# Optimization experiments

Hardware: AMD Instinct MI355X
Metric: run time of the kernel (lower is better)

Reference implementation:

```python
import jax, jax.numpy as jnp
import numpy as np

# regular 3x3 kernel grid: row0 = dy (i-1), row1 = dx (j-1), k = 3*i + j
RY = jnp.array([-1., -1., -1., 0., 0., 0., 1., 1., 1.], dtype=jnp.float32)
RX = jnp.array([-1., 0., 1., -1., 0., 1., -1., 0., 1.], dtype=jnp.float32)


def conv2d(x, w, b):
    # 3x3, stride 1, pad 1, NCHW/OIHW
    out = jax.lax.conv_general_dilated(
        x, w, window_strides=(1, 1), padding=((1, 1), (1, 1)),
        dimension_numbers=('NCHW', 'OIHW', 'NCHW'))
    return out + b[None, :, None, None]


def group_norm(x, gamma, beta, num_groups, eps=1e-5):
    N, C, H, W = x.shape
    xg = x.reshape(N, num_groups, C // num_groups, H, W)
    mu = xg.mean(axis=(2, 3, 4), keepdims=True)
    var = xg.var(axis=(2, 3, 4), keepdims=True)
    xn = ((xg - mu) * jax.lax.rsqrt(var + eps)).reshape(N, C, H, W)
    return xn * gamma[None, :, None, None] + beta[None, :, None, None]


def build_offset(tm, tr):
    # tm: [N,4,H,W] per-pixel 2x2 affine [[m00,m01],[m10,m11]]; tr: [N,2,H,W] (ty, tx)
    m00, m01, m10, m11 = tm[:, 0], tm[:, 1], tm[:, 2], tm[:, 3]  # [N,H,W]
    ry = RY[None, :, None, None]
    rx = RX[None, :, None, None]
    # offset = M @ R - R, plus translation broadcast to all 9 points
    dy = m00[:, None] * ry + m01[:, None] * rx - ry + tr[:, 0:1]  # [N,9,H,W]
    dx = m10[:, None] * ry + m11[:, None] * rx - rx + tr[:, 1:2]  # [N,9,H,W]
    return dy, dx


def bilinear_sample(img, py, px):
    # img: [N,C,H,W]; py, px: [N,K,H,W] sampling locations; zero padding outside
    N, C, H, W = img.shape
    K = py.shape[1]
    y0f = jnp.floor(py)
    x0f = jnp.floor(px)
    wy1 = py - y0f
    wx1 = px - x0f
    wy0 = 1.0 - wy1
    wx0 = 1.0 - wx1
    y0 = y0f.astype(jnp.int32)
    x0 = x0f.astype(jnp.int32)
    img_flat = img.reshape(N, C, H * W)

    def gather(yi, xi):
        valid = ((yi >= 0) & (yi < H) & (xi >= 0) & (xi < W)).astype(img.dtype)
        idx = jnp.clip(yi, 0, H - 1) * W + jnp.clip(xi, 0, W - 1)  # [N,K,H,W]
        flat = idx.reshape(N, 1, K * H * W)
        vals = jnp.take_along_axis(img_flat, jnp.broadcast_to(flat, (N, C, K * H * W)), axis=2)
        return vals.reshape(N, C, K, H, W) * valid[:, None]

    v00 = gather(y0, x0)
    v01 = gather(y0, x0 + 1)
    v10 = gather(y0 + 1, x0)
    v11 = gather(y0 + 1, x0 + 1)
    return (v00 * (wy0 * wx0)[:, None] + v01 * (wy0 * wx1)[:, None]
            + v10 * (wy1 * wx0)[:, None] + v11 * (wy1 * wx1)[:, None])


def deform_conv(x, dy, dx, w, pad=1, dil=1):
    # x: [N,Cin,H,W]; dy,dx: [N,9,H,W]; w: [Cout,Cin,3,3]; stride 1
    N, C, H, W = x.shape
    k = jnp.arange(9)
    ki = (k // 3).astype(x.dtype)[None, :, None, None]
    kj = (k % 3).astype(x.dtype)[None, :, None, None]
    hh = jnp.arange(H, dtype=x.dtype)[None, None, :, None]
    ww = jnp.arange(W, dtype=x.dtype)[None, None, None, :]
    py = hh - pad + dil * ki + dy  # [N,9,H,W]
    px = ww - pad + dil * kj + dx
    sampled = bilinear_sample(x, py, px)  # [N,C,9,H,W]
    return jnp.einsum('nckhw,ock->nohw', sampled, w.reshape(w.shape[0], C, 9))


def setup_inputs() -> dict:
    key = jax.random.key(0)
    ks = jax.random.split(key, 16)
    N, C, H, W = 4, 256, 64, 64
    x = jax.random.normal(ks[0], (N, C, H, W), jnp.float32)
    def p(k, shape, s):
        return jax.random.normal(k, shape, jnp.float32) * s
    s_off = 0.01                       # small STN heads -> modest offsets
    s_dc = 1.0 / np.sqrt(C * 9.0)      # deform-conv fan-in init
    return {
        'x': x,
        'w_tm1': p(ks[1], (4, C, 3, 3), s_off), 'b_tm1': jnp.zeros((4,), jnp.float32),
        'w_tr1': p(ks[2], (2, C, 3, 3), s_off), 'b_tr1': jnp.zeros((2,), jnp.float32),
        'w_dc1': p(ks[3], (C, C, 3, 3), s_dc),
        'g1': jnp.ones((C,), jnp.float32), 'be1': jnp.zeros((C,), jnp.float32),
        'w_tm2': p(ks[4], (4, C, 3, 3), s_off), 'b_tm2': jnp.zeros((4,), jnp.float32),
        'w_tr2': p(ks[5], (2, C, 3, 3), s_off), 'b_tr2': jnp.zeros((2,), jnp.float32),
        'w_dc2': p(ks[6], (C, C, 3, 3), s_dc),
        'g2': jnp.ones((C,), jnp.float32), 'be2': jnp.zeros((C,), jnp.float32),
    }


def reference(x, w_tm1, b_tm1, w_tr1, b_tr1, w_dc1, g1, be1,
              w_tm2, b_tm2, w_tr2, b_tr2, w_dc2, g2, be2):
    GROUPS = 32
    residual = x
    dy1, dx1 = build_offset(conv2d(x, w_tm1, b_tm1), conv2d(x, w_tr1, b_tr1))
    out = deform_conv(x, dy1, dx1, w_dc1)
    out = jax.nn.relu(group_norm(out, g1, be1, GROUPS))
    dy2, dx2 = build_offset(conv2d(out, w_tm2, b_tm2), conv2d(out, w_tr2, b_tr2))
    out = deform_conv(out, dy2, dx2, w_dc2)
    out = group_norm(out, g2, be2, GROUPS)
    return jax.nn.relu(out + residual)
```

## Files before the change

### kernel.cpp

```cpp
#include <hip/hip_runtime.h>


typedef unsigned int u32;
typedef unsigned short u16;
typedef __attribute__((ext_vector_type(8))) short bf16x8;
typedef __attribute__((ext_vector_type(4))) float floatx4;

#define HW 4096
#define CHW 1048576

static __device__ __forceinline__ float bf2f(u16 u) {
    union { u32 i; float f; } c; c.i = ((u32)u) << 16; return c.f;
}
static __device__ __forceinline__ u16 f2bf(float f) {
    union { float f; u32 i; } c; c.f = f;
    u32 x = c.i;
    return (u16)((x + 0x7FFFu + ((x >> 16) & 1u)) >> 16);
}
static __device__ __forceinline__ u32 cvtpk(float a, float b) {
    u32 r;
    asm("v_cvt_pk_bf16_f32 %0, %1, %2" : "=v"(r) : "v"(a), "v"(b));
    return r;
}
static __device__ __forceinline__ void lbar() {
    __builtin_amdgcn_sched_barrier(0);
    asm volatile("s_waitcnt lgkmcnt(0)" ::: "memory");
    __builtin_amdgcn_s_barrier();
    __builtin_amdgcn_sched_barrier(0);
}
static __device__ __forceinline__ float loadv(const void* p, long i, int f32) {
    return f32 ? ((const float*)p)[i] : bf2f(((const u16*)p)[i]);
}
static __device__ __forceinline__ int sniff_f32(const u32* __restrict__ xw) {
    int cnt = 0;
    #pragma unroll
    for (int s = 0; s < 16; ++s) {
        union { u32 i; float f; } c;
        c.i = xw[s * 131 + 7];
        float a = fabsf(c.f);
        if (a > 1e-8f && a < 1e4f) ++cnt;
    }
    return (cnt >= 8) ? 1 : 0;
}

__global__ __launch_bounds__(256) void k_prep_all(
    const void* __restrict__ x,
    const void* __restrict__ wdc1, const void* __restrict__ wdc2,
    const void* __restrict__ wtm1, const void* __restrict__ wtr1,
    const void* __restrict__ wtm2, const void* __restrict__ wtr2,
    u16* __restrict__ xT, u16* __restrict__ wTg1, u16* __restrict__ wTg2,
    u16* __restrict__ wT61, u16* __restrict__ wT62)
{
    __shared__ u16 T[64 * 258];
    const int f32 = sniff_f32((const u32*)x);
    const int b = blockIdx.x;
    const int tid = threadIdx.x;

    if (b < 256) {
        const int n = b >> 6, h = b & 63;
        const long sb = (long)n * CHW + (h << 6);
        const int cb = tid >> 3;
        const int w0 = (tid & 7) << 3;
        if (f32) {
            const float* xp = (const float*)x;
            for (int it = 0; it < 8; ++it) {
                int c = (it << 5) + cb;
                const float* pr = xp + sb + (long)c * HW + w0;
                float4 a = ((const float4*)pr)[0];
                float4 d = ((const float4*)pr)[1];
                T[(w0 + 0) * 258 + c] = f2bf(a.x);
                T[(w0 + 1) * 258 + c] = f2bf(a.y);
                T[(w0 + 2) * 258 + c] = f2bf(a.z);
                T[(w0 + 3) * 258 + c] = f2bf(a.w);
                T[(w0 + 4) * 258 + c] = f2bf(d.x);
                T[(w0 + 5) * 258 + c] = f2bf(d.y);
                T[(w0 + 6) * 258 + c] = f2bf(d.z);
                T[(w0 + 7) * 258 + c] = f2bf(d.w);
            }
        } else {
            const u16* xp = (const u16*)x;
            for (int it = 0; it < 8; ++it) {
                int c = (it << 5) + cb;
                uint4 v = *(const uint4*)(xp + sb + (long)c * HW + w0);
                u32 ws[4] = {v.x, v.y, v.z, v.w};
                #pragma unroll
                for (int q = 0; q < 4; ++q) {
                    T[(w0 + 2 * q + 0) * 258 + c] = (u16)(ws[q] & 0xFFFFu);
                    T[(w0 + 2 * q + 1) * 258 + c] = (u16)(ws[q] >> 16);
                }
            }
        }
        __syncthreads();
        const int w = tid >> 2, cq = tid & 3;
        const u32* Tr = (const u32*)T;
        u16* ob = xT + (long)n * CHW + (long)((h << 6) + w) * 256 + cq * 64;
        #pragma unroll
        for (int s = 0; s < 8; ++s) {
            uint4 o;
            o.x = Tr[129 * w + 32 * cq + 4 * s + 0];
            o.y = Tr[129 * w + 32 * cq + 4 * s + 1];
            o.z = Tr[129 * w + 32 * cq + 4 * s + 2];
            o.w = Tr[129 * w + 32 * cq + 4 * s + 3];
            *(uint4*)&ob[s * 8] = o;
        }
    } else if (b < 2560) {
        const int r2 = (b >= 1408);
        const void* wdc = r2 ? wdc2 : wdc1;
        u16* wTg = r2 ? wTg2 : wTg1;
        int idx2 = (b - (r2 ? 1408 : 256)) * 256 + tid;
        int cp = idx2 & 15;
        int o  = (idx2 >> 4) & 255;
        int q  = idx2 >> 12;
        int k  = q >> 3;
        int c0 = ((q & 7) << 5) + (cp << 1);
        long s0 = (long)o * 2304 + c0 * 9 + k;
        ((u32*)wTg)[idx2] = cvtpk(loadv(wdc, s0, f32), loadv(wdc, s0 + 9, f32));
    } else {
        const int r2 = (b >= 2704);
        const void* wtm = r2 ? wtm2 : wtm1;
        const void* wtr = r2 ? wtr2 : wtr1;
        u16* wT6 = r2 ? wT62 : wT61;
        int i = (b - (r2 ? 2704 : 2560)) * 256 + tid;
        int q  = i >> 9;
        int o  = (i >> 5) & 15;
        int cc = i & 31;
        int k  = q >> 3;
        int c  = ((q & 7) << 5) + cc;
        float v = 0.f;
        if (o < 4)      v = loadv(wtm, (long)o * 2304 + c * 9 + k, f32);
        else if (o < 6) v = loadv(wtr, (long)(o - 4) * 2304 + c * 9 + k, f32);
        wT6[i] = f2bf(v);
    }
}

__global__ __launch_bounds__(1024, 4) void k_deform(
    const u16* __restrict__ srcT, const u16* __restrict__ wTg,
    const u16* __restrict__ wT6,
    const void* __restrict__ b_tm, const void* __restrict__ b_tr,
    const u32* __restrict__ xw,
    u16* __restrict__ raw, float* __restrict__ pstats)
{
    __shared__ __align__(16) char shm[65536];
    __shared__ float tl[6 * 64];
    __shared__ int   g_y0[576];
    __shared__ int   g_x0[576];
    __shared__ float g_wy[576];
    __shared__ float g_wx[576];

    const int tid = threadIdx.x;
    const int bid = blockIdx.x;
    const int n = bid >> 6, h = bid & 63;
    const int lane = tid & 63;
    const int quad = lane >> 4;
    const int l16  = lane & 15;
    const int wv   = tid >> 6;
    const long nbase = (long)n * CHW;
    const u16* sp = srcT + nbase;

    {
        float (*red)[64][17] = (float (*)[64][17])shm;
        if (wv < 8) {
            floatx4 acc6[4];
            #pragma unroll
            for (int j = 0; j < 4; ++j) acc6[j] = (floatx4){0.f, 0.f, 0.f, 0.f};
            for (int qi = 0; qi < 9; ++qi) {
                const int q = wv * 9 + qi;
                const int k = q >> 3, cb = q & 7;
                const int ky = k / 3, kx = k % 3;
                const int row = h + ky - 1;
                const bool rv = (row >= 0) && (row < 64);
                bf16x8 av = *(const bf16x8*)&wT6[(((q << 4) + l16) << 5) + (quad << 3)];
                #pragma unroll
                for (int j = 0; j < 4; ++j) {
                    int psrc = (j << 4) + l16 + kx - 1;
                    bf16x8 bv = {0, 0, 0, 0, 0, 0, 0, 0};
                    if (rv && psrc >= 0 && psrc < 64)
                        bv = *(const bf16x8*)&sp[(((long)(row << 6) + psrc) << 8) + (cb << 5) + (quad << 3)];
                    acc6[j] = __builtin_amdgcn_mfma_f32_16x16x32_bf16(av, bv, acc6[j], 0, 0, 0);
                }
            }
            #pragma unroll
            for (int j = 0; j < 4; ++j)
                #pragma unroll
                for (int r = 0; r < 4; ++r)
                    red[wv][(j << 4) + l16][(quad << 2) + r] = acc6[j][r];
        }
        __syncthreads();
        if (tid < 384) {
            const int o = tid >> 6, px = tid & 63;
            float s = 0.f;
            #pragma unroll
            for (int v = 0; v < 8; ++v) s += red[v][px][o];
            const int f32 = sniff_f32(xw);
            float bias = (o < 4) ? loadv(b_tm, o, f32) : loadv(b_tr, o - 4, f32);
            tl[o * 64 + px] = s + bias;
        }
        __syncthreads();
    }

    if (tid < 576) {
        int i = tid;
        int k = i >> 6, ww2 = i & 63;
        float m00 = tl[ww2],        m01 = tl[64 + ww2];
        float m10 = tl[128 + ww2],  m11 = tl[192 + ww2];
        float tr0 = tl[256 + ww2],  tr1 = tl[320 + ww2];
        float ry = (float)(k / 3) - 1.f;
        float rx = (float)(k % 3) - 1.f;
        float dy = m00 * ry + m01 * rx - ry + tr0;
        float dx = m10 * ry + m11 * rx - rx + tr1;
        float py = (float)h + ry + dy;
        float px = (float)ww2 + rx + dx;
        float y0f = floorf(py), x0f = floorf(px);
        g_y0[i] = (int)y0f; g_x0[i] = (int)x0f;
        g_wy[i] = py - y0f; g_wx[i] = px - x0f;
    }
    __syncthreads();

    const int px   = tid >> 4;
    const int slot = tid & 15;
    const int o0   = wv << 4;
    const u32 xw_s = (u32)((px  & 7) << 2);
    const u32 xsw  = (u32)((l16 & 7) << 2);
    const u32 q4x  = (u32)(quad << 2);

    u32* Sl = (u32*)shm;

    floatx4 acc[4];
    #pragma unroll
    for (int g = 0; g < 4; ++g) acc[g] = (floatx4){0.f, 0.f, 0.f, 0.f};

    const int wlane = ((o0 + l16) << 5) + (quad << 3);
    const u16* wq = wTg;

    const u16 *p00, *p01, *p10, *p11;
    float cw00, cw01, cw10, cw11;

    auto mkptr = [&](int k) {
        int gi = (k << 6) + px;
        int y0 = g_y0[gi], x0 = g_x0[gi];
        int yc0 = min(max(y0, 0), 63),     yc1 = min(max(y0 + 1, 0), 63);
        int xc0 = min(max(x0, 0), 63),     xc1 = min(max(x0 + 1, 0), 63);
        const u16* bp = sp + (slot << 3);
        p00 = bp + (((yc0 << 6) + xc0) << 8);
        p01 = bp + (((yc0 << 6) + xc1) << 8);
        p10 = bp + (((yc1 << 6) + xc0) << 8);
        p11 = bp + (((yc1 << 6) + xc1) << 8);
    };
    auto mkcw = [&](int k) {
        int gi = (k << 6) + px;
        int y0 = g_y0[gi], x0 = g_x0[gi];
        float wy1 = g_wy[gi], wx1 = g_wx[gi];
        float wy0 = 1.f - wy1, wx0 = 1.f - wx1;
        bool yv0 = (y0 >= 0) && (y0 < 64);
        bool yv1 = (y0 >= -1) && (y0 < 63);
        bool xv0 = (x0 >= 0) && (x0 < 64);
        bool xv1 = (x0 >= -1) && (x0 < 63);
        cw00 = (yv0 && xv0) ? wy0 * wx0 : 0.f;
        cw01 = (yv0 && xv1) ? wy0 * wx1 : 0.f;
        cw10 = (yv1 && xv0) ? wy1 * wx0 : 0.f;
        cw11 = (yv1 && xv1) ? wy1 * wx1 : 0.f;
    };

    uint4 GA, GB, GC, GD, HA, HB, HC, HD;
    auto GATHER = [&]() {
        GA = *(const uint4*)(p00);  HA = *(const uint4*)(p00 + 128);
        GB = *(const uint4*)(p01);  HB = *(const uint4*)(p01 + 128);
        GC = *(const uint4*)(p10);  HC = *(const uint4*)(p10 + 128);
        GD = *(const uint4*)(p11);  HD = *(const uint4*)(p11 + 128);
    };

    bf16x8 W[4];
    auto WLD = [&](int s) {
        W[s] = *(const bf16x8*)(wq + wlane);
        wq += 8192;
    };

#define BIL(a, b, c, d) cvtpk( \
    fmaf(cw00, bf2f((u16)(a)), fmaf(cw01, bf2f((u16)(b)), \
    fmaf(cw10, bf2f((u16)(c)), cw11 * bf2f((u16)(d))))), \
    fmaf(cw00, bf2f((u16)((a) >> 16)), fmaf(cw01, bf2f((u16)((b) >> 16)), \
    fmaf(cw10, bf2f((u16)((c) >> 16)), cw11 * bf2f((u16)((d) >> 16))))))

    mkptr(0); GATHER();
    WLD(0); WLD(1);

    for (int k = 0; k < 9; ++k) {
        const int buf = k & 1;
        mkcw(k);
        uint4 v0 = make_uint4(BIL(GA.x, GB.x, GC.x, GD.x), BIL(GA.y, GB.y, GC.y, GD.y),
                              BIL(GA.z, GB.z, GC.z, GD.z), BIL(GA.w, GB.w, GC.w, GD.w));
        uint4 v1 = make_uint4(BIL(HA.x, HB.x, HC.x, HD.x), BIL(HA.y, HB.y, HC.y, HD.y),
                              BIL(HA.z, HB.z, HC.z, HD.z), BIL(HA.w, HB.w, HC.w, HD.w));
        u32* wp = &Sl[((u32)(buf << 13)) + ((u32)(px << 7)) + (((u32)(slot << 2)) ^ xw_s)];
        *(uint4*)wp = v0;
        *(uint4*)(wp + 64) = v1;
        if (k < 8) { mkptr(k + 1); GATHER(); }
        lbar();
        const u32* sb = &Sl[(u32)(buf << 13)];
        #pragma unroll
        for (int c = 0; c < 8; ++c) {
            const u32 offc = (((u32)(c << 4)) | q4x) ^ xsw;
            bf16x8 b0 = *(const bf16x8*)(sb + ((u32)(( 0 + l16) << 7)) + offc);
            bf16x8 b1 = *(const bf16x8*)(sb + ((u32)((16 + l16) << 7)) + offc);
            bf16x8 b2 = *(const bf16x8*)(sb + ((u32)((32 + l16) << 7)) + offc);
            bf16x8 b3 = *(const bf16x8*)(sb + ((u32)((48 + l16) << 7)) + offc);
            if (k < 8 || c < 6) WLD((c + 2) & 3);
            const int ws = c & 3;
            acc[0] = __builtin_amdgcn_mfma_f32_16x16x32_bf16(W[ws], b0, acc[0], 0, 0, 0);
            acc[1] = __builtin_amdgcn_mfma_f32_16x16x32_bf16(W[ws], b1, acc[1], 0, 0, 0);
            acc[2] = __builtin_amdgcn_mfma_f32_16x16x32_bf16(W[ws], b2, acc[2], 0, 0, 0);
            acc[3] = __builtin_amdgcn_mfma_f32_16x16x32_bf16(W[ws], b3, acc[3], 0, 0, 0);
        }
    }
#undef BIL

    {
        float s1 = 0.f, s2 = 0.f;
        #pragma unroll
        for (int g = 0; g < 4; ++g)
            #pragma unroll
            for (int r = 0; r < 4; ++r) {
                float v = acc[g][r];
                s1 += v; s2 += v * v;
            }
        #pragma unroll
        for (int off = 1; off <= 16; off <<= 1) {
            s1 += __shfl_xor(s1, off, 64);
            s2 += __shfl_xor(s2, off, 64);
        }
        if ((lane & 31) == 0) {
            int gg = (o0 >> 3) + (lane >> 5);
            pstats[((long)bid << 6) + (gg << 1)]     = s1;
            pstats[((long)bid << 6) + (gg << 1) + 1] = s2;
        }
    }

    #pragma unroll
    for (int g = 0; g < 4; ++g)
        #pragma unroll
        for (int r = 0; r < 4; ++r) {
            int o = o0 + quad * 4 + r;
            raw[nbase + ((long)o << 12) + (h << 6) + (g << 4) + l16]
                = f2bf(acc[g][r]);
        }
}

__global__ __launch_bounds__(256) void k_gn_relu(
    const u16* __restrict__ raw, const float* __restrict__ pstats,
    const void* __restrict__ gamma, const void* __restrict__ beta,
    const u32* __restrict__ xw,
    u16* __restrict__ out1)
{
    __shared__ u16 T[64 * 258];
    __shared__ float sred[4][64];
    __shared__ float sl[64];
    const int f32 = sniff_f32(xw);
    const int bid = blockIdx.x;
    const int n = bid >> 6, h = bid & 63;
    const int tid = threadIdx.x;

    {
        const int v = tid & 63, part = tid >> 6;
        float a = 0.f;
        for (int j = part * 16; j < part * 16 + 16; ++j)
            a += pstats[(((long)n * 64 + j) << 6) + v];
        sred[part][v] = a;
        __syncthreads();
        if (tid < 64) sl[tid] = sred[0][tid] + sred[1][tid] + sred[2][tid] + sred[3][tid];
        __syncthreads();
    }

    const u16* rb = raw + (long)n * CHW + (h << 6);
    const int cb = tid >> 3;
    const int w0 = (tid & 7) << 3;
    for (int it = 0; it < 8; ++it) {
        int c = (it << 5) + cb;
        int g = c >> 3;
        float mean = sl[g * 2] * (1.f / 32768.f);
        float var  = sl[g * 2 + 1] * (1.f / 32768.f) - mean * mean;
        float rstd = rsqrtf(var + 1e-5f);
        float ga = loadv(gamma, c, f32) * rstd;
        float be = loadv(beta, c, f32) - mean * ga;
        uint4 v = *(const uint4*)(rb + (long)c * HW + w0);
        u32 ws[4] = {v.x, v.y, v.z, v.w};
        #pragma unroll
        for (int q = 0; q < 4; ++q) {
            float a = fmaxf(fmaf(bf2f((u16)(ws[q] & 0xFFFFu)), ga, be), 0.f);
            float b = fmaxf(fmaf(bf2f((u16)(ws[q] >> 16)),     ga, be), 0.f);
            T[(w0 + 2 * q + 0) * 258 + c] = f2bf(a);
            T[(w0 + 2 * q + 1) * 258 + c] = f2bf(b);
        }
    }
    __syncthreads();
    const int w = tid >> 2, cq = tid & 3;
    const u32* Tr = (const u32*)T;
    u16* ob = out1 + (long)n * CHW + (long)((h << 6) + w) * 256 + cq * 64;
    #pragma unroll
    for (int s = 0; s < 8; ++s) {
        uint4 o;
        o.x = Tr[129 * w + 32 * cq + 4 * s + 0];
        o.y = Tr[129 * w + 32 * cq + 4 * s + 1];
        o.z = Tr[129 * w + 32 * cq + 4 * s + 2];
        o.w = Tr[129 * w + 32 * cq + 4 * s + 3];
        *(uint4*)&ob[s * 8] = o;
    }
}

__global__ __launch_bounds__(256) void k_gn_final(
    const u16* __restrict__ raw, const float* __restrict__ pstats,
    const void* __restrict__ gamma, const void* __restrict__ beta,
    const void* __restrict__ x,
    void* __restrict__ outp)
{
    __shared__ float rr[256];
    const int f32 = sniff_f32((const u32*)x);
    const int tid = threadIdx.x;
    const long e0 = ((long)blockIdx.x) << 11;
    const int n = (int)(e0 >> 20);
    const int c0 = (int)((e0 >> 12) & 255);
    const int g = c0 >> 3;

    {
        int j = tid & 127, sv = tid >> 7;
        rr[tid] = (j < 64) ? pstats[(((long)n * 64 + j) << 6) + (g << 1) + sv] : 0.f;
        __syncthreads();
        #pragma unroll
        for (int s = 64; s >= 1; s >>= 1) {
            if ((tid & 127) < s) rr[tid] += rr[tid + s];
            __syncthreads();
        }
    }
    float mean = rr[0] * (1.f / 32768.f);
    float var  = rr[128] * (1.f / 32768.f) - mean * mean;
    float rstd = rsqrtf(var + 1e-5f);

    const long i = blockIdx.x * 256 + tid;
    const long e = i << 3;
    const int c = (int)((e >> 12) & 255);
    float ga = loadv(gamma, c, f32) * rstd;
    float be = loadv(beta, c, f32) - mean * ga;
    uint4 p = ((const uint4*)raw)[i];
    u32 ww[4] = {p.x, p.y, p.z, p.w};
    float v[8];
    #pragma unroll
    for (int q = 0; q < 4; ++q) {
        v[2 * q + 0] = fmaxf(fmaf(bf2f((u16)(ww[q] & 0xFFFFu)), ga, be) + loadv(x, e + 2 * q + 0, f32), 0.f);
        v[2 * q + 1] = fmaxf(fmaf(bf2f((u16)(ww[q] >> 16)),     ga, be) + loadv(x, e + 2 * q + 1, f32), 0.f);
    }
    if (f32) {
        float4* op = (float4*)((float*)outp + e);
        op[0] = make_float4(v[0], v[1], v[2], v[3]);
        op[1] = make_float4(v[4], v[5], v[6], v[7]);
    } else {
        uint4 o;
        o.x = cvtpk(v[0], v[1]);
        o.y = cvtpk(v[2], v[3]);
        o.z = cvtpk(v[4], v[5]);
        o.w = cvtpk(v[6], v[7]);
        ((uint4*)outp)[i] = o;
    }
}

extern "C" void kernel_launch(void* const* d_in, const int* in_sizes, int n_in,
                              void* d_out, int out_size, void* d_ws, size_t ws_size,
                              hipStream_t stream) {
    const void* x     = d_in[0];
    const void* w_tm1 = d_in[1];
    const void* b_tm1 = d_in[2];
    const void* w_tr1 = d_in[3];
    const void* b_tr1 = d_in[4];
    const void* w_dc1 = d_in[5];
    const void* g1    = d_in[6];
    const void* be1   = d_in[7];
    const void* w_tm2 = d_in[8];
    const void* b_tm2 = d_in[9];
    const void* w_tr2 = d_in[10];
    const void* b_tr2 = d_in[11];
    const void* w_dc2 = d_in[12];
    const void* g2    = d_in[13];
    const void* be2   = d_in[14];

    char* wsb = (char*)d_ws;
    u16*   xT     = (u16*)wsb;
    u16*   raw    = (u16*)(wsb + 8388608);
    u16*   wTg1   = (u16*)(wsb + 16777216);
    u16*   wTg2   = (u16*)(wsb + 17956864);
    u16*   wT61   = (u16*)(wsb + 19136512);
    u16*   wT62   = (u16*)(wsb + 19210240);
    float* pstats = (float*)(wsb + 19283968);
    u16*   out1   = xT;
    const u32* xw = (const u32*)x;

    k_prep_all<<<2848, 256, 0, stream>>>(x, w_dc1, w_dc2, w_tm1, w_tr1, w_tm2, w_tr2,
                                         xT, wTg1, wTg2, wT61, wT62);
    k_deform  <<<256, 1024, 0, stream>>>(xT, wTg1, wT61, b_tm1, b_tr1, xw, raw, pstats);
    k_gn_relu <<<256, 256, 0, stream>>>(raw, pstats, g1, be1, xw, out1);
    k_deform  <<<256, 1024, 0, stream>>>(out1, wTg2, wT62, b_tm2, b_tr2, xw, raw, pstats);
    k_gn_final<<<2048, 256, 0, stream>>>(raw, pstats, g2, be2, x, d_out);
}
```

Measured before the change: 221.6 us.

## Split K across wave halves with 32-channel output tiles and LDS reduction

```diff
diff --git a/kernel.cpp b/kernel.cpp
--- a/kernel.cpp
+++ b/kernel.cpp
@@ -218,33 +218,37 @@
 
     const int px   = tid >> 4;
     const int slot = tid & 15;
-    const int o0   = wv << 4;
+    const int kh   = wv >> 3;
+    const int o0   = (wv & 7) << 5;
     const u32 xw_s = (u32)((px  & 7) << 2);
     const u32 xsw  = (u32)((l16 & 7) << 2);
     const u32 q4x  = (u32)(quad << 2);
+    const u32 kh64 = (u32)(kh << 6);
 
     u32* Sl = (u32*)shm;
 
-    floatx4 acc[4];
+    floatx4 acc[2][4];
     #pragma unroll
-    for (int g = 0; g < 4; ++g) acc[g] = (floatx4){0.f, 0.f, 0.f, 0.f};
+    for (int a = 0; a < 2; ++a)
+        #pragma unroll
+        for (int g = 0; g < 4; ++g) acc[a][g] = (floatx4){0.f, 0.f, 0.f, 0.f};
 
     const int wlane = ((o0 + l16) << 5) + (quad << 3);
-    const u16* wq = wTg;
-
-    const u16 *p00, *p01, *p10, *p11;
+    const u16* wk = wTg + (kh << 15);
+
+    u32 o00, o01, o10, o11;
     float cw00, cw01, cw10, cw11;
+    const char* spb = (const char*)sp + (slot << 4);
 
     auto mkptr = [&](int k) {
         int gi = (k << 6) + px;
         int y0 = g_y0[gi], x0 = g_x0[gi];
         int yc0 = min(max(y0, 0), 63),     yc1 = min(max(y0 + 1, 0), 63);
         int xc0 = min(max(x0, 0), 63),     xc1 = min(max(x0 + 1, 0), 63);
-        const u16* bp = sp + (slot << 3);
-        p00 = bp + (((yc0 << 6) + xc0) << 8);
-        p01 = bp + (((yc0 << 6) + xc1) << 8);
-        p10 = bp + (((yc1 << 6) + xc0) << 8);
-        p11 = bp + (((yc1 << 6) + xc1) << 8);
+        o00 = (u32)(((yc0 << 6) + xc0) << 9);
+        o01 = (u32)(((yc0 << 6) + xc1) << 9);
+        o10 = (u32)(((yc1 << 6) + xc0) << 9);
+        o11 = (u32)(((yc1 << 6) + xc1) << 9);
     };
     auto mkcw = [&](int k) {
         int gi = (k << 6) + px;
@@ -263,17 +267,13 @@
 
     uint4 GA, GB, GC, GD, HA, HB, HC, HD;
     auto GATHER = [&]() {
-        GA = *(const uint4*)(p00);  HA = *(const uint4*)(p00 + 128);
-        GB = *(const uint4*)(p01);  HB = *(const uint4*)(p01 + 128);
-        GC = *(const uint4*)(p10);  HC = *(const uint4*)(p10 + 128);
-        GD = *(const uint4*)(p11);  HD = *(const uint4*)(p11 + 128);
+        GA = *(const uint4*)(spb + o00);  HA = *(const uint4*)(spb + o00 + 256);
+        GB = *(const uint4*)(spb + o01);  HB = *(const uint4*)(spb + o01 + 256);
+        GC = *(const uint4*)(spb + o10);  HC = *(const uint4*)(spb + o10 + 256);
+        GD = *(const uint4*)(spb + o11);  HD = *(const uint4*)(spb + o11 + 256);
     };
 
-    bf16x8 W[4];
-    auto WLD = [&](int s) {
-        W[s] = *(const bf16x8*)(wq + wlane);
-        wq += 8192;
-    };
+    bf16x8 W0[4], W1[4];
 
 #define BIL(a, b, c, d) cvtpk( \
     fmaf(cw00, bf2f((u16)(a)), fmaf(cw01, bf2f((u16)(b)), \
@@ -282,7 +282,10 @@
     fmaf(cw10, bf2f((u16)((c) >> 16)), cw11 * bf2f((u16)((d) >> 16))))))
 
     mkptr(0); GATHER();
-    WLD(0); WLD(1);
+    W0[0] = *(const bf16x8*)(wk + wlane);
+    W1[0] = *(const bf16x8*)(wk + wlane + 512);
+    W0[1] = *(const bf16x8*)(wk + 8192 + wlane);
+    W1[1] = *(const bf16x8*)(wk + 8192 + wlane + 512);
 
     for (int k = 0; k < 9; ++k) {
         const int buf = k & 1;
@@ -298,51 +301,87 @@
         lbar();
         const u32* sb = &Sl[(u32)(buf << 13)];
         #pragma unroll
-        for (int c = 0; c < 8; ++c) {
-            const u32 offc = (((u32)(c << 4)) | q4x) ^ xsw;
+        for (int c = 0; c < 4; ++c) {
+            const u32 offc = (((kh64 + (u32)(c << 4))) | q4x) ^ xsw;
             bf16x8 b0 = *(const bf16x8*)(sb + ((u32)(( 0 + l16) << 7)) + offc);
             bf16x8 b1 = *(const bf16x8*)(sb + ((u32)((16 + l16) << 7)) + offc);
             bf16x8 b2 = *(const bf16x8*)(sb + ((u32)((32 + l16) << 7)) + offc);
             bf16x8 b3 = *(const bf16x8*)(sb + ((u32)((48 + l16) << 7)) + offc);
-            if (k < 8 || c < 6) WLD((c + 2) & 3);
-            const int ws = c & 3;
-            acc[0] = __builtin_amdgcn_mfma_f32_16x16x32_bf16(W[ws], b0, acc[0], 0, 0, 0);
-            acc[1] = __builtin_amdgcn_mfma_f32_16x16x32_bf16(W[ws], b1, acc[1], 0, 0, 0);
-            acc[2] = __builtin_amdgcn_mfma_f32_16x16x32_bf16(W[ws], b2, acc[2], 0, 0, 0);
-            acc[3] = __builtin_amdgcn_mfma_f32_16x16x32_bf16(W[ws], b3, acc[3], 0, 0, 0);
-        }
+            if (k < 8 || c < 2) {
+                const int tc = c + 2;
+                const u16* wb = wk + ((tc & 3) + ((tc >> 2) << 3)) * 8192;
+                W0[tc & 3] = *(const bf16x8*)(wb + wlane);
+                W1[tc & 3] = *(const bf16x8*)(wb + wlane + 512);
+            }
+            acc[0][0] = __builtin_amdgcn_mfma_f32_16x16x32_bf16(W0[c], b0, acc[0][0], 0, 0, 0);
+            acc[0][1] = __builtin_amdgcn_mfma_f32_16x16x32_bf16(W0[c], b1, acc[0][1], 0, 0, 0);
+            acc[0][2] = __builtin_amdgcn_mfma_f32_16x16x32_bf16(W0[c], b2, acc[0][2], 0, 0, 0);
+            acc[0][3] = __builtin_amdgcn_mfma_f32_16x16x32_bf16(W0[c], b3, acc[0][3], 0, 0, 0);
+            acc[1][0] = __builtin_amdgcn_mfma_f32_16x16x32_bf16(W1[c], b0, acc[1][0], 0, 0, 0);
+            acc[1][1] = __builtin_amdgcn_mfma_f32_16x16x32_bf16(W1[c], b1, acc[1][1], 0, 0, 0);
+            acc[1][2] = __builtin_amdgcn_mfma_f32_16x16x32_bf16(W1[c], b2, acc[1][2], 0, 0, 0);
+            acc[1][3] = __builtin_amdgcn_mfma_f32_16x16x32_bf16(W1[c], b3, acc[1][3], 0, 0, 0);
+        }
+        wk += 65536;
     }
 #undef BIL
 
+    __syncthreads();
     {
-        float s1 = 0.f, s2 = 0.f;
-        #pragma unroll
-        for (int g = 0; g < 4; ++g)
-            #pragma unroll
-            for (int r = 0; r < 4; ++r) {
-                float v = acc[g][r];
-                s1 += v; s2 += v * v;
+        float* ms = (float*)shm;
+        if (kh == 1) {
+            #pragma unroll
+            for (int a = 0; a < 2; ++a)
+                #pragma unroll
+                for (int g = 0; g < 4; ++g)
+                    *(floatx4*)&ms[((((wv & 7) << 3) + (a << 2) + g) << 8) + (lane << 2)] = acc[a][g];
+        }
+        __syncthreads();
+        if (kh == 0) {
+            #pragma unroll
+            for (int a = 0; a < 2; ++a)
+                #pragma unroll
+                for (int g = 0; g < 4; ++g) {
+                    floatx4 t = *(const floatx4*)&ms[((((wv & 7) << 3) + (a << 2) + g) << 8) + (lane << 2)];
+                    acc[a][g] += t;
+                }
+        }
+    }
+
+    if (kh == 0) {
+        #pragma unroll
+        for (int a = 0; a < 2; ++a) {
+            float s1 = 0.f, s2 = 0.f;
+            #pragma unroll
+            for (int g = 0; g < 4; ++g)
+                #pragma unroll
+                for (int r = 0; r < 4; ++r) {
+                    float v = acc[a][g][r];
+                    s1 += v; s2 += v * v;
+                }
+            #pragma unroll
+            for (int off = 1; off <= 16; off <<= 1) {
+                s1 += __shfl_xor(s1, off, 64);
+                s2 += __shfl_xor(s2, off, 64);
             }
-        #pragma unroll
-        for (int off = 1; off <= 16; off <<= 1) {
-            s1 += __shfl_xor(s1, off, 64);
-            s2 += __shfl_xor(s2, off, 64);
-        }
-        if ((lane & 31) == 0) {
-            int gg = (o0 >> 3) + (lane >> 5);
-            pstats[((long)bid << 6) + (gg << 1)]     = s1;
-            pstats[((long)bid << 6) + (gg << 1) + 1] = s2;
-        }
-    }
-
-    #pragma unroll
-    for (int g = 0; g < 4; ++g)
-        #pragma unroll
-        for (int r = 0; r < 4; ++r) {
-            int o = o0 + quad * 4 + r;
-            raw[nbase + ((long)o << 12) + (h << 6) + (g << 4) + l16]
-                = f2bf(acc[g][r]);
-        }
+            if ((lane & 31) == 0) {
+                int gg = (o0 >> 3) + (a << 1) + (lane >> 5);
+                pstats[((long)bid << 6) + (gg << 1)]     = s1;
+                pstats[((long)bid << 6) + (gg << 1) + 1] = s2;
+            }
+        }
+
+        #pragma unroll
+        for (int a = 0; a < 2; ++a)
+            #pragma unroll
+            for (int g = 0; g < 4; ++g)
+                #pragma unroll
+                for (int r = 0; r < 4; ++r) {
+                    int o = o0 + (a << 4) + (quad << 2) + r;
+                    raw[nbase + ((long)o << 12) + (h << 6) + (g << 4) + l16]
+                        = f2bf(acc[a][g][r]);
+                }
+    }
 }
 
 __global__ __launch_bounds__(256) void k_gn_relu(
```

Result: faster. 214.3 us (-3.3%).
